# Performance work log

Hardware: AMD Instinct MI355X
Metric: run time of the kernel (lower is better)

Reference implementation:

```python
import jax, jax.numpy as jnp
import numpy as np

N_R = 100_000   # real nodes
N_E = 1_200_000 # r2r edges
G = 4096        # graphs (= interaction nodes, one per graph)
H = 64          # hidden_dim
ND = 64         # node_dim
ED = 16         # edge_dim
L = 4           # conv_layers
TGT = 1         # target_dim
SLOPE = 0.1     # LeakyReLU negative slope used by ISATconv


def _seg_softmax(logits, seg, n):
    m = jax.ops.segment_max(logits, seg, num_segments=n)
    ex = jnp.exp(logits - m[seg])
    s = jax.ops.segment_sum(ex, seg, num_segments=n)
    return ex / s[seg]


def setup_inputs() -> dict:
    key = jax.random.key(0)
    ks = jax.random.split(key, 20)
    inp = {}
    inp['r_node'] = jax.random.normal(ks[0], (N_R, ND), jnp.float32)
    inp['i_node'] = jax.random.normal(ks[1], (G, 1), jnp.float32)
    inp['r_edge'] = jax.random.normal(ks[2], (N_E, ED), jnp.float32)
    inp['d_edge'] = jax.random.uniform(ks[3], (N_R, 1), jnp.float32)
    inp['r2r_src'] = jax.random.randint(ks[4], (N_E,), 0, N_R, jnp.int32)
    inp['r2r_dst'] = jax.random.randint(ks[5], (N_E,), 0, N_R, jnp.int32)
    inp['graph_id'] = jnp.sort(jax.random.randint(ks[6], (N_R,), 0, G, jnp.int32))
    sc = 1.0 / np.sqrt(H)
    inp['W_r'] = jax.random.normal(ks[7], (ND, H), jnp.float32) * (1.0 / np.sqrt(ND))
    inp['W_i'] = jax.random.normal(ks[8], (1, H), jnp.float32)
    inp['W_e'] = jax.random.normal(ks[9], (ED, H), jnp.float32) * (1.0 / np.sqrt(ED))
    inp['Wm'] = jax.random.normal(ks[10], (L, H, H), jnp.float32) * sc
    inp['a_s'] = jax.random.normal(ks[11], (L, H), jnp.float32) * sc
    inp['a_d'] = jax.random.normal(ks[12], (L, H), jnp.float32) * sc
    inp['a_e'] = jax.random.normal(ks[13], (L, H), jnp.float32) * sc
    inp['w_d'] = jax.random.normal(ks[14], (1,), jnp.float32)
    inp['b_d'] = jnp.zeros((1,), jnp.float32)
    inp['W_mlp'] = jax.random.normal(ks[15], (3, H, H), jnp.float32) * sc
    inp['b_mlp'] = jnp.zeros((3, H), jnp.float32)
    inp['W_out'] = jax.random.normal(ks[16], (H, TGT), jnp.float32) * sc
    inp['b_out'] = jnp.zeros((TGT,), jnp.float32)
    return inp


def reference(r_node, i_node, r_edge, d_edge, r2r_src, r2r_dst, graph_id,
              W_r, W_i, W_e, Wm, a_s, a_d, a_e, w_d, b_d,
              W_mlp, b_mlp, W_out, b_out):
    lrelu = lambda x: jax.nn.leaky_relu(x, SLOPE)
    n = r_node.shape[0]
    g = i_node.shape[0]
    # embeddings (bias-free linears)
    h = r_node @ W_r          # [N,H]
    hi = i_node @ W_i         # [G,H]
    e = r_edge @ W_e          # [E,H]
    score = None
    # ISAT attention conv layers (gather-compute-scatter), residual
    for l in range(L):
        logits = lrelu(h[r2r_src] @ a_s[l] + h[r2r_dst] @ a_d[l] + e @ a_e[l])  # [E]
        attn = _seg_softmax(logits, r2r_dst, n)
        msg = attn[:, None] * (h[r2r_src] + e)
        agg = jax.ops.segment_sum(msg, r2r_dst, num_segments=n) @ Wm[l]
        h = lrelu(h + agg)
        score = attn
    # interaction-node (d2d) mixing: gate by d_edge, gather to i-nodes, broadcast back
    gate = jax.nn.sigmoid(d_edge * w_d + b_d)                 # [N,1]
    hi = hi + jax.ops.segment_sum(gate * h, graph_id, num_segments=g)
    h = h + gate * hi[graph_id]
    # sum pooling over real-node subgraph per graph
    pooled = jax.ops.segment_sum(h, graph_id, num_segments=g)  # [G,H]
    # MLP readout: 3 hidden ReLU layers + linear output
    x = pooled
    for i in range(3):
        x = jax.nn.relu(x @ W_mlp[i] + b_mlp[i])
    return x @ W_out + b_out
```

## Files before the change

### kernel.cpp

```cpp
#include <hip/hip_runtime.h>
#include <math.h>

#define N_RN 100000
#define N_ED 1200000
#define N_G  4096
#define SCAN_CH 256
#define SCAN_NB ((N_RN + SCAN_CH - 1) / SCAN_CH)

__device__ __forceinline__ float lrelu(float x) { return x > 0.f ? x : 0.1f * x; }

__global__ void k_embed_h(const float* __restrict__ r_node,
                          const float* __restrict__ W_r,
                          const float* __restrict__ a_s0,
                          const float* __restrict__ a_d0,
                          float* __restrict__ h,
                          float* __restrict__ hs, float* __restrict__ hd) {
    __shared__ float Wl[64 * 64];
    __shared__ float arow[4][64];
    int tid = threadIdx.x;
    for (int i = tid; i < 4096; i += 256) Wl[i] = W_r[i];
    __syncthreads();
    int lane = tid & 63, w = tid >> 6;
    float asj = a_s0[lane], adj = a_d0[lane];
    int wid = blockIdx.x * 4 + w;
    int nw = gridDim.x * 4;
    for (int n = wid; n < N_RN; n += nw) {
        arow[w][lane] = r_node[(size_t)n * 64 + lane];
        float acc = 0.f;
#pragma unroll
        for (int d4 = 0; d4 < 16; ++d4) {
            float4 a = *(const float4*)&arow[w][d4 * 4];
            int d = d4 * 4;
            acc += a.x * Wl[(d + 0) * 64 + lane];
            acc += a.y * Wl[(d + 1) * 64 + lane];
            acc += a.z * Wl[(d + 2) * 64 + lane];
            acc += a.w * Wl[(d + 3) * 64 + lane];
        }
        h[(size_t)n * 64 + lane] = acc;
        float x = acc * asj, y = acc * adj;
#pragma unroll
        for (int off = 32; off; off >>= 1) {
            x += __shfl_xor(x, off, 64);
            y += __shfl_xor(y, off, 64);
        }
        if (lane == 0) { hs[n] = x; hd[n] = y; }
    }
}

__global__ void k_wewm(const float* __restrict__ W_e,
                       const float* __restrict__ Wm,
                       const float* __restrict__ a_e,
                       float* __restrict__ WeWm,
                       float* __restrict__ was_all) {
    int idx = blockIdx.x * blockDim.x + threadIdx.x;
    if (idx < 4096) {
        int l = idx >> 10, rem = idx & 1023;
        int t = rem >> 6, j = rem & 63;
        float acc = 0.f;
        for (int d = 0; d < 64; ++d)
            acc += W_e[t * 64 + d] * Wm[l * 4096 + d * 64 + j];
        WeWm[idx] = acc;
    } else {
        int r = idx - 4096;
        if (r < 64) {
            int l = r >> 4, t = r & 15;
            float acc = 0.f;
            for (int j = 0; j < 64; ++j)
                acc += W_e[t * 64 + j] * a_e[l * 64 + j];
            was_all[r] = acc;
        }
    }
}

__global__ void k_hist(const int* __restrict__ dst, int* __restrict__ deg) {
    int k = blockIdx.x * blockDim.x + threadIdx.x;
    if (k < N_ED) atomicAdd(deg + dst[k], 1);
}

__global__ void k_scan_a(const int* __restrict__ deg, int* __restrict__ bsum) {
    __shared__ int lds[SCAN_CH];
    int b = blockIdx.x, t = threadIdx.x;
    int i = b * SCAN_CH + t;
    int v = (i < N_RN) ? deg[i] : 0;
    lds[t] = v;
    __syncthreads();
    for (int d = 128; d; d >>= 1) {
        if (t < d) lds[t] += lds[t + d];
        __syncthreads();
    }
    if (t == 0) bsum[b] = lds[0];
}

__global__ void k_scan_b(int* __restrict__ bsum) {
    __shared__ int lds[512];
    int t = threadIdx.x;
    int v = (t < SCAN_NB) ? bsum[t] : 0;
    lds[t] = v;
    __syncthreads();
    for (int d = 1; d < 512; d <<= 1) {
        int u = (t >= d) ? lds[t - d] : 0;
        __syncthreads();
        lds[t] += u;
        __syncthreads();
    }
    if (t < SCAN_NB) bsum[t] = lds[t] - v;
}

__global__ void k_scan_c(const int* __restrict__ deg, const int* __restrict__ bsum,
                         int* __restrict__ off, int* __restrict__ cur) {
    __shared__ int lds[SCAN_CH];
    int b = blockIdx.x, t = threadIdx.x;
    int i = b * SCAN_CH + t;
    int v = (i < N_RN) ? deg[i] : 0;
    lds[t] = v;
    __syncthreads();
    for (int d = 1; d < SCAN_CH; d <<= 1) {
        int u = (t >= d) ? lds[t - d] : 0;
        __syncthreads();
        lds[t] += u;
        __syncthreads();
    }
    if (i < N_RN) {
        int incl = bsum[b] + lds[t];
        off[i + 1] = incl;
        cur[i] = incl - v;
        if (i == 0) off[0] = 0;
    }
}

__global__ void k_scatter(const float* __restrict__ r_edge,
                          const int* __restrict__ src, const int* __restrict__ dst,
                          int* __restrict__ cur,
                          int* __restrict__ src_perm,
                          float* __restrict__ r16_perm) {
    int k = blockIdx.x * blockDim.x + threadIdx.x;
    if (k >= N_ED) return;
    const float4* row = (const float4*)(r_edge + (size_t)k * 16);
    float4 r0 = row[0], r1 = row[1], r2 = row[2], r3 = row[3];
    int pos = atomicAdd(cur + dst[k], 1);
    src_perm[pos] = src[k];
    float4* o = (float4*)(r16_perm + (size_t)pos * 16);
    o[0] = r0; o[1] = r1; o[2] = r2; o[3] = r3;
}

__global__ void k_layer(const float* __restrict__ h_in,
                        const float* __restrict__ hs, const float* __restrict__ hd,
                        const int* __restrict__ off,
                        const int* __restrict__ src_perm,
                        const float* __restrict__ r16_perm,
                        const float* __restrict__ was_l,
                        const float* __restrict__ Wm_l,
                        const float* __restrict__ WeWm_l,
                        const float* __restrict__ a_s_n, const float* __restrict__ a_d_n,
                        float* __restrict__ h_out,
                        float* __restrict__ hs_out, float* __restrict__ hd_out) {
    __shared__ float Wl[4096];
    __shared__ float Ww[1024];
    __shared__ float arow[8][4 * 68 + 4];
    int tid = threadIdx.x;
    for (int i = tid; i < 4096; i += 512) Wl[i] = Wm_l[i];
    for (int i = tid; i < 1024; i += 512) Ww[i] = WeWm_l[i];
    __syncthreads();
    int lane = tid & 63, w = tid >> 6;
    int g = lane >> 4, lg = lane & 15;
    float wr[16];
#pragma unroll
    for (int t = 0; t < 16; ++t) wr[t] = was_l[t];
    float4 as4 = *(const float4*)&a_s_n[lg << 2];
    float4 ad4 = *(const float4*)&a_d_n[lg << 2];
    int Wv = blockIdx.x * 8 + w;
    int NW = gridDim.x * 8;
    for (int nb = Wv * 4; nb < N_RN; nb += NW * 4) {
        int n = nb + g;
        bool nact = n < N_RN;
        int base = 0, end = 0;
        if (nact) { base = off[n]; end = off[n + 1]; }
        float hdn = nact ? hd[n] : 0.f;
        float m = -1e38f, s = 0.f, racc = 0.f;
        float ax = 0.f, ay = 0.f, az = 0.f, aw = 0.f;
        int nch = (end - base + 15) >> 4;
        int nmax = nch;
        nmax = max(nmax, __shfl_xor(nmax, 16, 64));
        nmax = max(nmax, __shfl_xor(nmax, 32, 64));
        for (int c = 0; c < nmax; ++c) {
            int cb = base + (c << 4);
            int rem = end - cb;
            int cnt = rem > 16 ? 16 : (rem > 0 ? rem : 0);
            float lgt = -1e38f;
            float wvv = 0.f;
            int sk = 0;
            bool act = lg < cnt;
            if (act) {
                int pos = cb + lg;
                sk = src_perm[pos];
                const float4* rp = (const float4*)(r16_perm + (size_t)pos * 16);
                float4 r0 = rp[0], r1 = rp[1], r2 = rp[2], r3 = rp[3];
                float ep = r0.x * wr[0] + r0.y * wr[1] + r0.z * wr[2] + r0.w * wr[3]
                         + r1.x * wr[4] + r1.y * wr[5] + r1.z * wr[6] + r1.w * wr[7]
                         + r2.x * wr[8] + r2.y * wr[9] + r2.z * wr[10] + r2.w * wr[11]
                         + r3.x * wr[12] + r3.y * wr[13] + r3.z * wr[14] + r3.w * wr[15];
                lgt = lrelu(hs[sk] + hdn + ep);
            }
            float cm = lgt;
            cm = fmaxf(cm, __shfl_xor(cm, 1, 16));
            cm = fmaxf(cm, __shfl_xor(cm, 2, 16));
            cm = fmaxf(cm, __shfl_xor(cm, 4, 16));
            cm = fmaxf(cm, __shfl_xor(cm, 8, 16));
            float newm = fmaxf(m, cm);
            float scale = (m > -1e37f) ? __expf(m - newm) : 0.f;
            s *= scale; racc *= scale;
            ax *= scale; ay *= scale; az *= scale; aw *= scale;
            m = newm;
            if (act) wvv = __expf(lgt - m);
            s += wvv;
            int e = 0;
            for (; e + 1 < cnt; e += 2) {
                float wgt0 = __shfl(wvv, e, 16);
                int   sk0  = __shfl(sk, e, 16);
                float wgt1 = __shfl(wvv, e + 1, 16);
                int   sk1  = __shfl(sk, e + 1, 16);
                const float4 h0v = *(const float4*)(h_in + (size_t)sk0 * 64 + (lg << 2));
                const float4 h1v = *(const float4*)(h_in + (size_t)sk1 * 64 + (lg << 2));
                float q0 = r16_perm[(size_t)(cb + e) * 16 + lg];
                float q1 = r16_perm[(size_t)(cb + e + 1) * 16 + lg];
                ax += wgt0 * h0v.x + wgt1 * h1v.x;
                ay += wgt0 * h0v.y + wgt1 * h1v.y;
                az += wgt0 * h0v.z + wgt1 * h1v.z;
                aw += wgt0 * h0v.w + wgt1 * h1v.w;
                racc += wgt0 * q0 + wgt1 * q1;
            }
            if (e < cnt) {
                float wgt0 = __shfl(wvv, e, 16);
                int   sk0  = __shfl(sk, e, 16);
                const float4 h0v = *(const float4*)(h_in + (size_t)sk0 * 64 + (lg << 2));
                float q0 = r16_perm[(size_t)(cb + e) * 16 + lg];
                ax += wgt0 * h0v.x; ay += wgt0 * h0v.y;
                az += wgt0 * h0v.z; aw += wgt0 * h0v.w;
                racc += wgt0 * q0;
            }
        }
        s += __shfl_xor(s, 1, 16);
        s += __shfl_xor(s, 2, 16);
        s += __shfl_xor(s, 4, 16);
        s += __shfl_xor(s, 8, 16);
        float inv = (end > base) ? 1.f / s : 0.f;
        float* ar = &arow[w][g * 68];
        *(float4*)&ar[lg << 2] = make_float4(ax * inv, ay * inv, az * inv, aw * inv);
        float mx = 0.f, my = 0.f, mz = 0.f, mw = 0.f;
#pragma unroll
        for (int d4 = 0; d4 < 16; ++d4) {
            float4 a = *(const float4*)&ar[d4 << 2];
            const float* wl = &Wl[(d4 << 2) * 64 + (lg << 2)];
            float4 w0 = *(const float4*)&wl[0];
            float4 w1 = *(const float4*)&wl[64];
            float4 w2 = *(const float4*)&wl[128];
            float4 w3 = *(const float4*)&wl[192];
            mx += a.x * w0.x + a.y * w1.x + a.z * w2.x + a.w * w3.x;
            my += a.x * w0.y + a.y * w1.y + a.z * w2.y + a.w * w3.y;
            mz += a.x * w0.z + a.y * w1.z + a.z * w2.z + a.w * w3.z;
            mw += a.x * w0.w + a.y * w1.w + a.z * w2.w + a.w * w3.w;
        }
        float rs = racc * inv;
#pragma unroll
        for (int t = 0; t < 16; ++t) {
            float rt = __shfl(rs, t, 16);
            const float4 wt = *(const float4*)&Ww[t * 64 + (lg << 2)];
            mx += rt * wt.x; my += rt * wt.y; mz += rt * wt.z; mw += rt * wt.w;
        }
        if (nact) {
            const float4 hi4 = *(const float4*)(h_in + (size_t)n * 64 + (lg << 2));
            float4 hv;
            hv.x = lrelu(hi4.x + mx); hv.y = lrelu(hi4.y + my);
            hv.z = lrelu(hi4.z + mz); hv.w = lrelu(hi4.w + mw);
            *(float4*)(h_out + (size_t)n * 64 + (lg << 2)) = hv;
            float x = hv.x * as4.x + hv.y * as4.y + hv.z * as4.z + hv.w * as4.w;
            float y = hv.x * ad4.x + hv.y * ad4.y + hv.z * ad4.z + hv.w * ad4.w;
            x += __shfl_xor(x, 1, 16); x += __shfl_xor(x, 2, 16);
            x += __shfl_xor(x, 4, 16); x += __shfl_xor(x, 8, 16);
            y += __shfl_xor(y, 1, 16); y += __shfl_xor(y, 2, 16);
            y += __shfl_xor(y, 4, 16); y += __shfl_xor(y, 8, 16);
            if (lg == 0) { hs_out[n] = x; hd_out[n] = y; }
        }
    }
}

__global__ void k_readout(const float* __restrict__ h,
                          const float* __restrict__ d_edge,
                          const int* __restrict__ graph_id,
                          const float* __restrict__ i_node,
                          const float* __restrict__ W_i,
                          const float* __restrict__ w_d,
                          const float* __restrict__ b_d,
                          const float* __restrict__ W_mlp,
                          const float* __restrict__ b_mlp,
                          const float* __restrict__ W_out,
                          const float* __restrict__ b_out,
                          float* __restrict__ out) {
    int g = blockIdx.x, j = threadIdx.x;
    int lo = 0, hi = N_RN;
    while (lo < hi) { int mid = (lo + hi) >> 1; if (graph_id[mid] < g) lo = mid + 1; else hi = mid; }
    int start = lo;
    hi = N_RN;
    while (lo < hi) { int mid = (lo + hi) >> 1; if (graph_id[mid] < g + 1) lo = mid + 1; else hi = mid; }
    int end = lo;

    float wd = w_d[0], bd = b_d[0];
    float acc0 = 0.f, acc1 = 0.f, sg = 0.f;
    for (int n = start; n < end; ++n) {
        float hv = h[(size_t)n * 64 + j];
        float de = d_edge[n];
        float gate = 1.f / (1.f + __expf(-(de * wd + bd)));
        acc0 += hv;
        acc1 += gate * hv;
        sg += gate;
    }
    float hij = i_node[g] * W_i[j] + acc1;
    float pooled = acc0 + sg * hij;

    __shared__ float xa[64], xb[64];
    xa[j] = pooled;
    __syncthreads();
#pragma unroll
    for (int layer = 0; layer < 3; ++layer) {
        const float* W = W_mlp + layer * 4096;
        float* srcb = (layer & 1) ? xb : xa;
        float* dstb = (layer & 1) ? xa : xb;
        float acc = b_mlp[layer * 64 + j];
        for (int d = 0; d < 64; ++d) acc += srcb[d] * W[d * 64 + j];
        acc = fmaxf(acc, 0.f);
        __syncthreads();
        dstb[j] = acc;
        __syncthreads();
    }
    float v = xb[j] * W_out[j];
#pragma unroll
    for (int off = 32; off; off >>= 1) v += __shfl_xor(v, off, 64);
    if (j == 0) out[g] = v + b_out[0];
}

extern "C" void kernel_launch(void* const* d_in, const int* in_sizes, int n_in,
                              void* d_out, int out_size, void* d_ws, size_t ws_size,
                              hipStream_t stream) {
    const float* r_node  = (const float*)d_in[0];
    const float* i_node  = (const float*)d_in[1];
    const float* r_edge  = (const float*)d_in[2];
    const float* d_edge  = (const float*)d_in[3];
    const int*   r2r_src = (const int*)d_in[4];
    const int*   r2r_dst = (const int*)d_in[5];
    const int*   graph_id= (const int*)d_in[6];
    const float* W_r     = (const float*)d_in[7];
    const float* W_i     = (const float*)d_in[8];
    const float* W_e     = (const float*)d_in[9];
    const float* Wm      = (const float*)d_in[10];
    const float* a_s     = (const float*)d_in[11];
    const float* a_d     = (const float*)d_in[12];
    const float* a_e     = (const float*)d_in[13];
    const float* w_d     = (const float*)d_in[14];
    const float* b_d     = (const float*)d_in[15];
    const float* W_mlp   = (const float*)d_in[16];
    const float* b_mlp   = (const float*)d_in[17];
    const float* W_out   = (const float*)d_in[18];
    const float* b_out   = (const float*)d_in[19];
    float* out = (float*)d_out;

    float* ws = (float*)d_ws;
    float* h0   = ws;
    float* h1   = h0 + (size_t)N_RN * 64;
    float* hs0  = h1 + (size_t)N_RN * 64;
    float* hd0  = hs0 + N_RN;
    float* hs1  = hd0 + N_RN;
    float* hd1  = hs1 + N_RN;
    float* WeWm = hd1 + N_RN;
    float* wasb = WeWm + 4096;
    int*   deg  = (int*)(wasb + 64);
    int*   offs = deg + N_RN;
    int*   cur  = offs + N_RN + 1;
    int*   bsum = cur + N_RN;
    int*   src_perm = bsum + 512;
    float* r16_perm = (float*)(src_perm + N_ED);

    k_embed_h<<<2048, 256, 0, stream>>>(r_node, W_r, a_s, a_d, h0, hs0, hd0);
    k_wewm<<<17, 256, 0, stream>>>(W_e, Wm, a_e, WeWm, wasb);

    hipMemsetAsync(deg, 0, N_RN * sizeof(int), stream);
    k_hist<<<(N_ED + 255) / 256, 256, 0, stream>>>(r2r_dst, deg);
    k_scan_a<<<SCAN_NB, SCAN_CH, 0, stream>>>(deg, bsum);
    k_scan_b<<<1, 512, 0, stream>>>(bsum);
    k_scan_c<<<SCAN_NB, SCAN_CH, 0, stream>>>(deg, bsum, offs, cur);
    k_scatter<<<(N_ED + 255) / 256, 256, 0, stream>>>(r_edge, r2r_src, r2r_dst,
                                                      cur, src_perm, r16_perm);

    float* hin = h0;  float* hout = h1;
    float* hsi = hs0; float* hdi = hd0;
    float* hso = hs1; float* hdo = hd1;
    for (int l = 0; l < 4; ++l) {
        int ln = (l + 1) & 3;
        k_layer<<<1024, 512, 0, stream>>>(hin, hsi, hdi, offs, src_perm, r16_perm,
                                          wasb + l * 16, Wm + l * 4096, WeWm + l * 1024,
                                          a_s + ln * 64, a_d + ln * 64,
                                          hout, hso, hdo);
        float* t;
        t = hin; hin = hout; hout = t;
        t = hsi; hsi = hso; hso = t;
        t = hdi; hdi = hdo; hdo = t;
    }

    k_readout<<<N_G, 64, 0, stream>>>(hin, d_edge, graph_id, i_node, W_i, w_d, b_d,
                                      W_mlp, b_mlp, W_out, b_out, out);
}
```

Baseline: 729.6 us.

## Add dynamic work stealing, split edge scatter into index and permute passes, unroll gather by 4

The layer kernel now takes node groups from a per-layer global atomic counter instead of a fixed grid stride, which balances work across warps when node degrees vary. Edge sorting is split into a small atomic pass that writes only edge indices and a second pass that gathers src and edge features into sorted order, so the wide 64-byte writes become coalesced. The inner aggregation loop is unrolled from 2 to 4 edges to keep more gather loads in flight. The cost is one extra kernel launch and index buffer, one atomic per warp iteration, and higher register pressure.

```diff
diff --git a/kernel.cpp b/kernel.cpp
--- a/kernel.cpp
+++ b/kernel.cpp
@@ -128,17 +128,26 @@
     }
 }
 
-__global__ void k_scatter(const float* __restrict__ r_edge,
-                          const int* __restrict__ src, const int* __restrict__ dst,
-                          int* __restrict__ cur,
+__global__ void k_scatter_idx(const int* __restrict__ dst,
+                              int* __restrict__ cur,
+                              int* __restrict__ eperm) {
+    int k = blockIdx.x * blockDim.x + threadIdx.x;
+    if (k >= N_ED) return;
+    int pos = atomicAdd(cur + dst[k], 1);
+    eperm[pos] = k;
+}
+
+__global__ void k_permute(const int* __restrict__ eperm,
+                          const int* __restrict__ src,
+                          const float* __restrict__ r_edge,
                           int* __restrict__ src_perm,
                           float* __restrict__ r16_perm) {
-    int k = blockIdx.x * blockDim.x + threadIdx.x;
-    if (k >= N_ED) return;
+    int pos = blockIdx.x * blockDim.x + threadIdx.x;
+    if (pos >= N_ED) return;
+    int k = eperm[pos];
+    src_perm[pos] = src[k];
     const float4* row = (const float4*)(r_edge + (size_t)k * 16);
     float4 r0 = row[0], r1 = row[1], r2 = row[2], r3 = row[3];
-    int pos = atomicAdd(cur + dst[k], 1);
-    src_perm[pos] = src[k];
     float4* o = (float4*)(r16_perm + (size_t)pos * 16);
     o[0] = r0; o[1] = r1; o[2] = r2; o[3] = r3;
 }
@@ -152,6 +161,7 @@
                         const float* __restrict__ Wm_l,
                         const float* __restrict__ WeWm_l,
                         const float* __restrict__ a_s_n, const float* __restrict__ a_d_n,
+                        int* __restrict__ ctr,
                         float* __restrict__ h_out,
                         float* __restrict__ hs_out, float* __restrict__ hd_out) {
     __shared__ float Wl[4096];
@@ -170,8 +180,9 @@
     float4 ad4 = *(const float4*)&a_d_n[lg << 2];
     int Wv = blockIdx.x * 8 + w;
     int NW = gridDim.x * 8;
-    for (int nb = Wv * 4; nb < N_RN; nb += NW * 4) {
-        int n = nb + g;
+    int it = Wv;
+    while (it * 4 < N_RN) {
+        int n = it * 4 + g;
         bool nact = n < N_RN;
         int base = 0, end = 0;
         if (nact) { base = off[n]; end = off[n + 1]; }
@@ -213,30 +224,39 @@
             m = newm;
             if (act) wvv = __expf(lgt - m);
             s += wvv;
+            const float* hb = h_in;
             int e = 0;
-            for (; e + 1 < cnt; e += 2) {
-                float wgt0 = __shfl(wvv, e, 16);
-                int   sk0  = __shfl(sk, e, 16);
-                float wgt1 = __shfl(wvv, e + 1, 16);
-                int   sk1  = __shfl(sk, e + 1, 16);
-                const float4 h0v = *(const float4*)(h_in + (size_t)sk0 * 64 + (lg << 2));
-                const float4 h1v = *(const float4*)(h_in + (size_t)sk1 * 64 + (lg << 2));
+            for (; e + 3 < cnt; e += 4) {
+                float w0 = __shfl(wvv, e, 16);
+                float w1 = __shfl(wvv, e + 1, 16);
+                float w2 = __shfl(wvv, e + 2, 16);
+                float w3 = __shfl(wvv, e + 3, 16);
+                int   s0 = __shfl(sk, e, 16);
+                int   s1 = __shfl(sk, e + 1, 16);
+                int   s2 = __shfl(sk, e + 2, 16);
+                int   s3 = __shfl(sk, e + 3, 16);
+                const float4 h0v = *(const float4*)(hb + (size_t)s0 * 64 + (lg << 2));
+                const float4 h1v = *(const float4*)(hb + (size_t)s1 * 64 + (lg << 2));
+                const float4 h2v = *(const float4*)(hb + (size_t)s2 * 64 + (lg << 2));
+                const float4 h3v = *(const float4*)(hb + (size_t)s3 * 64 + (lg << 2));
                 float q0 = r16_perm[(size_t)(cb + e) * 16 + lg];
                 float q1 = r16_perm[(size_t)(cb + e + 1) * 16 + lg];
-                ax += wgt0 * h0v.x + wgt1 * h1v.x;
-                ay += wgt0 * h0v.y + wgt1 * h1v.y;
-                az += wgt0 * h0v.z + wgt1 * h1v.z;
-                aw += wgt0 * h0v.w + wgt1 * h1v.w;
-                racc += wgt0 * q0 + wgt1 * q1;
+                float q2 = r16_perm[(size_t)(cb + e + 2) * 16 + lg];
+                float q3 = r16_perm[(size_t)(cb + e + 3) * 16 + lg];
+                ax += w0 * h0v.x + w1 * h1v.x + w2 * h2v.x + w3 * h3v.x;
+                ay += w0 * h0v.y + w1 * h1v.y + w2 * h2v.y + w3 * h3v.y;
+                az += w0 * h0v.z + w1 * h1v.z + w2 * h2v.z + w3 * h3v.z;
+                aw += w0 * h0v.w + w1 * h1v.w + w2 * h2v.w + w3 * h3v.w;
+                racc += w0 * q0 + w1 * q1 + w2 * q2 + w3 * q3;
             }
-            if (e < cnt) {
-                float wgt0 = __shfl(wvv, e, 16);
-                int   sk0  = __shfl(sk, e, 16);
-                const float4 h0v = *(const float4*)(h_in + (size_t)sk0 * 64 + (lg << 2));
+            for (; e < cnt; ++e) {
+                float w0 = __shfl(wvv, e, 16);
+                int   s0 = __shfl(sk, e, 16);
+                const float4 h0v = *(const float4*)(hb + (size_t)s0 * 64 + (lg << 2));
                 float q0 = r16_perm[(size_t)(cb + e) * 16 + lg];
-                ax += wgt0 * h0v.x; ay += wgt0 * h0v.y;
-                az += wgt0 * h0v.z; aw += wgt0 * h0v.w;
-                racc += wgt0 * q0;
+                ax += w0 * h0v.x; ay += w0 * h0v.y;
+                az += w0 * h0v.z; aw += w0 * h0v.w;
+                racc += w0 * q0;
             }
         }
         s += __shfl_xor(s, 1, 16);
@@ -281,6 +301,9 @@
             y += __shfl_xor(y, 4, 16); y += __shfl_xor(y, 8, 16);
             if (lg == 0) { hs_out[n] = x; hd_out[n] = y; }
         }
+        int itn = 0;
+        if (lane == 0) itn = atomicAdd(ctr, 1);
+        it = NW + __shfl(itn, 0, 64);
     }
 }
 
@@ -376,19 +399,23 @@
     int*   offs = deg + N_RN;
     int*   cur  = offs + N_RN + 1;
     int*   bsum = cur + N_RN;
-    int*   src_perm = bsum + 512;
+    int*   ctr  = bsum + 512;
+    int*   eperm= ctr + 4;
+    int*   src_perm = eperm + N_ED;
     float* r16_perm = (float*)(src_perm + N_ED);
 
     k_embed_h<<<2048, 256, 0, stream>>>(r_node, W_r, a_s, a_d, h0, hs0, hd0);
     k_wewm<<<17, 256, 0, stream>>>(W_e, Wm, a_e, WeWm, wasb);
 
     hipMemsetAsync(deg, 0, N_RN * sizeof(int), stream);
+    hipMemsetAsync(ctr, 0, 4 * sizeof(int), stream);
     k_hist<<<(N_ED + 255) / 256, 256, 0, stream>>>(r2r_dst, deg);
     k_scan_a<<<SCAN_NB, SCAN_CH, 0, stream>>>(deg, bsum);
     k_scan_b<<<1, 512, 0, stream>>>(bsum);
     k_scan_c<<<SCAN_NB, SCAN_CH, 0, stream>>>(deg, bsum, offs, cur);
-    k_scatter<<<(N_ED + 255) / 256, 256, 0, stream>>>(r_edge, r2r_src, r2r_dst,
-                                                      cur, src_perm, r16_perm);
+    k_scatter_idx<<<(N_ED + 255) / 256, 256, 0, stream>>>(r2r_dst, cur, eperm);
+    k_permute<<<(N_ED + 255) / 256, 256, 0, stream>>>(eperm, r2r_src, r_edge,
+                                                      src_perm, r16_perm);
 
     float* hin = h0;  float* hout = h1;
     float* hsi = hs0; float* hdi = hd0;
@@ -397,7 +424,7 @@
         int ln = (l + 1) & 3;
         k_layer<<<1024, 512, 0, stream>>>(hin, hsi, hdi, offs, src_perm, r16_perm,
                                           wasb + l * 16, Wm + l * 4096, WeWm + l * 1024,
-                                          a_s + ln * 64, a_d + ln * 64,
+                                          a_s + ln * 64, a_d + ln * 64, ctr + l,
                                           hout, hso, hdo);
         float* t;
         t = hin; hin = hout; hout = t;
```

After: 1.675 ms. +129.5%, slower.
